# Performance work log

Hardware: AMD Instinct MI355X
Metric: run time of the kernel (lower is better)

Reference implementation:

```python
import jax, jax.numpy as jnp
import numpy as np


def setup_inputs() -> dict:
    key = jax.random.key(0)
    k1, k2, k3, k4 = jax.random.split(key, 4)
    in_features, out_features = 4096, 11008
    n_tokens = 64
    x = jax.random.normal(k1, (n_tokens, in_features), dtype=jnp.float32)
    # int8-valued weights stored as int32 (values in [-128, 127] range subset)
    weight_int = jax.random.randint(k2, (out_features, in_features), 0, 127, dtype=jnp.int32)
    weight_scale = jnp.float32(0.01)
    weight_zero_point = 3  # scalar int zero point
    bias = jax.random.normal(k3, (out_features,), dtype=jnp.float32) * 0.02
    return {
        "x": x,
        "weight_int": weight_int,
        "weight_scale": weight_scale,
        "weight_zero_point": weight_zero_point,
        "bias": bias,
    }


def reference(x, weight_int, weight_scale, weight_zero_point, bias):
    # Dequantize: W = (W_int - zp) * scale, shape [out, in]
    w = (weight_int.astype(jnp.float32) - jnp.float32(weight_zero_point)) * weight_scale
    # F.linear: y = x @ W^T + b
    out = jnp.einsum("ti,oi->to", x, w)
    return out + bias
```

## Files before the change

### kernel.cpp

```cpp
#include <hip/hip_runtime.h>
#include <hip/hip_bf16.h>

typedef __attribute__((ext_vector_type(8))) short short8;
typedef __attribute__((ext_vector_type(4))) float f32x4;
typedef __attribute__((ext_vector_type(4))) int   int4v;

#define IN_F   4096
#define OUT_F  11008
#define KSPLIT 4
#define KPART  (IN_F / KSPLIT)
#define BK     64
#define NIT    (KPART / BK)
#define DEPTH  3

__device__ __forceinline__ short bf16_rne(float f) {
    unsigned u = __builtin_bit_cast(unsigned, f);
    u += 0x7FFFu + ((u >> 16) & 1u);
    return (short)(u >> 16);
}

__device__ __forceinline__ void gld16(const void* g, void* l) {
    __builtin_amdgcn_global_load_lds(
        (const __attribute__((address_space(1))) unsigned int*)g,
        (__attribute__((address_space(3))) unsigned int*)l,
        16, 0, 0);
}

__device__ __forceinline__ short8 deq8(int4v q0, int4v q1, int zp) {
    short8 r;
#pragma unroll
    for (int j = 0; j < 4; ++j) {
        r[j]     = (short)(__builtin_bit_cast(unsigned, (float)(q0[j] - zp)) >> 16);
        r[j + 4] = (short)(__builtin_bit_cast(unsigned, (float)(q1[j] - zp)) >> 16);
    }
    return r;
}

__global__ __launch_bounds__(256)
void xcast(const float* __restrict__ x, unsigned short* __restrict__ xb) {
    const int i = (blockIdx.x * 256 + threadIdx.x) * 8;
    f32x4 a = *(const f32x4*)(x + i);
    f32x4 b = *(const f32x4*)(x + i + 4);
    short8 o;
#pragma unroll
    for (int j = 0; j < 4; ++j) { o[j] = bf16_rne(a[j]); o[j + 4] = bf16_rne(b[j]); }
    *(short8*)(xb + i) = o;
}

__global__ __launch_bounds__(256)
void binit(const float* __restrict__ bias, float* __restrict__ out) {
    const unsigned cid = blockIdx.x * 256 + threadIdx.x;
    const unsigned row = cid / (OUT_F / 8);
    const unsigned o   = (cid - row * (OUT_F / 8)) * 8;
    f32x4 b0 = *(const f32x4*)(bias + o);
    f32x4 b1 = *(const f32x4*)(bias + o + 4);
    float* dst = out + (size_t)row * OUT_F + o;
    *(f32x4*)dst = b0;
    *(f32x4*)(dst + 4) = b1;
}

#define STAGE(IT) do {                                                        \
    const int _s = (IT) % DEPTH;                                              \
    const int* _wsi = wsrc + (size_t)(IT) * BK;                               \
    gld16(_wsi,              (char*)wt[_s] + tid * 16);                       \
    gld16(_wsi + 16 * IN_F,  (char*)wt[_s] + 4096  + tid * 16);               \
    gld16(_wsi + 32 * IN_F,  (char*)wt[_s] + 8192  + tid * 16);               \
    gld16(_wsi + 48 * IN_F,  (char*)wt[_s] + 12288 + tid * 16);               \
    const unsigned short* _xsi = xsrc + (size_t)(IT) * BK;                    \
    gld16(_xsi,            (char*)xt[_s] + tid * 16);                         \
    gld16(_xsi + 32 * IN_F, (char*)xt[_s] + 4096 + tid * 16);                 \
} while (0)

#define COMPUTE(S) do {                                                       \
    const char* _wb = (const char*)wt[S] + wrow_off;                          \
    int4v _q00 = *(const int4v*)(_wb + cw00);                                 \
    int4v _q01 = *(const int4v*)(_wb + cw01);                                 \
    int4v _q10 = *(const int4v*)(_wb + cw10);                                 \
    int4v _q11 = *(const int4v*)(_wb + cw11);                                 \
    short8 _B0 = deq8(_q00, _q01, zp);                                        \
    short8 _B1 = deq8(_q10, _q11, zp);                                        \
    const char* _xb = (const char*)xt[S] + arow;                              \
    short8 _a;                                                                \
    _a = *(const short8*)(_xb +        ca0);                                  \
    acc0 = __builtin_amdgcn_mfma_f32_16x16x32_bf16(_a, _B0, acc0, 0, 0, 0);   \
    _a = *(const short8*)(_xb +        ca1);                                  \
    acc0 = __builtin_amdgcn_mfma_f32_16x16x32_bf16(_a, _B1, acc0, 0, 0, 0);   \
    _a = *(const short8*)(_xb + 2048 + ca0);                                  \
    acc1 = __builtin_amdgcn_mfma_f32_16x16x32_bf16(_a, _B0, acc1, 0, 0, 0);   \
    _a = *(const short8*)(_xb + 2048 + ca1);                                  \
    acc1 = __builtin_amdgcn_mfma_f32_16x16x32_bf16(_a, _B1, acc1, 0, 0, 0);   \
    _a = *(const short8*)(_xb + 4096 + ca0);                                  \
    acc2 = __builtin_amdgcn_mfma_f32_16x16x32_bf16(_a, _B0, acc2, 0, 0, 0);   \
    _a = *(const short8*)(_xb + 4096 + ca1);                                  \
    acc2 = __builtin_amdgcn_mfma_f32_16x16x32_bf16(_a, _B1, acc2, 0, 0, 0);   \
    _a = *(const short8*)(_xb + 6144 + ca0);                                  \
    acc3 = __builtin_amdgcn_mfma_f32_16x16x32_bf16(_a, _B0, acc3, 0, 0, 0);   \
    _a = *(const short8*)(_xb + 6144 + ca1);                                  \
    acc3 = __builtin_amdgcn_mfma_f32_16x16x32_bf16(_a, _B1, acc3, 0, 0, 0);   \
} while (0)

__global__ __launch_bounds__(256, 2)
void qlin6(const unsigned short* __restrict__ xb, const int* __restrict__ w,
           const float* __restrict__ scale_p, const int* __restrict__ zp_p,
           float* __restrict__ out)
{
    __shared__ __align__(16) int            wt[DEPTH][64 * BK];
    __shared__ __align__(16) unsigned short xt[DEPTH][64 * BK];

    const int tid  = threadIdx.x;
    const int lane = tid & 63;
    const int wv   = tid >> 6;
    const int l15  = lane & 15;
    const int lg   = lane >> 4;

    const int ob = blockIdx.x >> 2;
    const int kh = blockIdx.x & 3;
    const int o0 = ob * 64;
    const int kb = kh * KPART;

    const int   zp    = zp_p[0];
    const float scale = scale_p[0];

    const int wr = tid >> 4;
    const int wc = (tid & 15) ^ (wr & 7);
    const int* wsrc = w + (size_t)(o0 + wr) * IN_F + kb + wc * 4;

    const int xr = tid >> 3;
    const int xc = (tid & 7) ^ (xr & 7);
    const unsigned short* xsrc = xb + (size_t)xr * IN_F + kb + xc * 8;

    const int rswz = l15 & 7;
    const int wrow_off = (wv * 16 + l15) * 256;
    const int cw00 = ((lg * 2    ) ^ rswz) * 16;
    const int cw01 = ((lg * 2 + 1) ^ rswz) * 16;
    const int cw10 = ((8 + lg * 2    ) ^ rswz) * 16;
    const int cw11 = ((8 + lg * 2 + 1) ^ rswz) * 16;
    const int arow = l15 * 128;
    const int ca0  = ((lg    ) ^ rswz) * 16;
    const int ca1  = ((4 + lg) ^ rswz) * 16;

    f32x4 acc0 = {0.f, 0.f, 0.f, 0.f};
    f32x4 acc1 = {0.f, 0.f, 0.f, 0.f};
    f32x4 acc2 = {0.f, 0.f, 0.f, 0.f};
    f32x4 acc3 = {0.f, 0.f, 0.f, 0.f};

    STAGE(0);
    STAGE(1);

#pragma unroll 3
    for (int it = 0; it < NIT - 1; ++it) {
        asm volatile("s_waitcnt vmcnt(6)" ::: "memory");
        __builtin_amdgcn_s_barrier();
        if (it + 2 < NIT) STAGE(it + 2);
        COMPUTE(it % DEPTH);
    }
    asm volatile("s_waitcnt vmcnt(0)" ::: "memory");
    __builtin_amdgcn_s_barrier();
    COMPUTE((NIT - 1) % DEPTH);

    {
        const int o = o0 + wv * 16 + l15;
        float* op = out + o;
#pragma unroll
        for (int r = 0; r < 4; ++r) {
            const int tr = lg * 4 + r;
            unsafeAtomicAdd(op + (size_t)(tr     ) * OUT_F, scale * acc0[r]);
            unsafeAtomicAdd(op + (size_t)(tr + 16) * OUT_F, scale * acc1[r]);
            unsafeAtomicAdd(op + (size_t)(tr + 32) * OUT_F, scale * acc2[r]);
            unsafeAtomicAdd(op + (size_t)(tr + 48) * OUT_F, scale * acc3[r]);
        }
    }
}

extern "C" void kernel_launch(void* const* d_in, const int* in_sizes, int n_in,
                              void* d_out, int out_size, void* d_ws, size_t ws_size,
                              hipStream_t stream) {
    const float* x     = (const float*)d_in[0];
    const int*   w     = (const int*)d_in[1];
    const float* scale = (const float*)d_in[2];
    const int*   zp    = (const int*)d_in[3];
    const float* bias  = (const float*)d_in[4];
    float*       out   = (float*)d_out;
    unsigned short* xbf = (unsigned short*)d_ws;

    xcast<<<dim3(128), dim3(256), 0, stream>>>(x, xbf);
    binit<<<dim3(344), dim3(256), 0, stream>>>(bias, out);
    qlin6<<<dim3((OUT_F / 64) * KSPLIT), dim3(256), 0, stream>>>(xbf, w, scale, zp, out);
}
```

Before: 47.97 us.

## Widen output tile to 128 columns, split K eight ways, merge prep kernels

Each block now runs 512 threads over 128 output columns, so one x tile staged in shared memory serves twice as many weight rows. K is split eight ways instead of four, giving more blocks for the weight stream. The shared-memory pipeline drops from triple to double buffering, with an extra barrier before each refill. The x cast and bias init are merged into one prep kernel, saving a launch. In exchange the kernel issues twice as many float atomics to the output, uses more shared memory per block, and has shorter K loops.

```diff
diff --git a/kernel.cpp b/kernel.cpp
--- a/kernel.cpp
+++ b/kernel.cpp
@@ -7,11 +7,12 @@
 
 #define IN_F   4096
 #define OUT_F  11008
-#define KSPLIT 4
+#define COLS   128
+#define KSPLIT 8
 #define KPART  (IN_F / KSPLIT)
 #define BK     64
 #define NIT    (KPART / BK)
-#define DEPTH  3
+#define DEPTH  2
 
 __device__ __forceinline__ short bf16_rne(float f) {
     unsigned u = __builtin_bit_cast(unsigned, f);
@@ -37,19 +38,18 @@
 }
 
 __global__ __launch_bounds__(256)
-void xcast(const float* __restrict__ x, unsigned short* __restrict__ xb) {
-    const int i = (blockIdx.x * 256 + threadIdx.x) * 8;
-    f32x4 a = *(const f32x4*)(x + i);
-    f32x4 b = *(const f32x4*)(x + i + 4);
-    short8 o;
+void prep(const float* __restrict__ x, const float* __restrict__ bias,
+          unsigned short* __restrict__ xb, float* __restrict__ out) {
+    const unsigned cid = blockIdx.x * 256 + threadIdx.x;
+    if (blockIdx.x < 128) {
+        const int i = cid * 8;
+        f32x4 a = *(const f32x4*)(x + i);
+        f32x4 b = *(const f32x4*)(x + i + 4);
+        short8 o;
 #pragma unroll
-    for (int j = 0; j < 4; ++j) { o[j] = bf16_rne(a[j]); o[j + 4] = bf16_rne(b[j]); }
-    *(short8*)(xb + i) = o;
-}
-
-__global__ __launch_bounds__(256)
-void binit(const float* __restrict__ bias, float* __restrict__ out) {
-    const unsigned cid = blockIdx.x * 256 + threadIdx.x;
+        for (int j = 0; j < 4; ++j) { o[j] = bf16_rne(a[j]); o[j + 4] = bf16_rne(b[j]); }
+        *(short8*)(xb + i) = o;
+    }
     const unsigned row = cid / (OUT_F / 8);
     const unsigned o   = (cid - row * (OUT_F / 8)) * 8;
     f32x4 b0 = *(const f32x4*)(bias + o);
@@ -60,15 +60,13 @@
 }
 
 #define STAGE(IT) do {                                                        \
-    const int _s = (IT) % DEPTH;                                              \
+    const int _s = (IT) & (DEPTH - 1);                                        \
     const int* _wsi = wsrc + (size_t)(IT) * BK;                               \
-    gld16(_wsi,              (char*)wt[_s] + tid * 16);                       \
-    gld16(_wsi + 16 * IN_F,  (char*)wt[_s] + 4096  + tid * 16);               \
-    gld16(_wsi + 32 * IN_F,  (char*)wt[_s] + 8192  + tid * 16);               \
-    gld16(_wsi + 48 * IN_F,  (char*)wt[_s] + 12288 + tid * 16);               \
-    const unsigned short* _xsi = xsrc + (size_t)(IT) * BK;                    \
-    gld16(_xsi,            (char*)xt[_s] + tid * 16);                         \
-    gld16(_xsi + 32 * IN_F, (char*)xt[_s] + 4096 + tid * 16);                 \
+    gld16(_wsi,             (char*)wt[_s] + tid * 16);                        \
+    gld16(_wsi + 32 * IN_F, (char*)wt[_s] + 8192  + tid * 16);                \
+    gld16(_wsi + 64 * IN_F, (char*)wt[_s] + 16384 + tid * 16);                \
+    gld16(_wsi + 96 * IN_F, (char*)wt[_s] + 24576 + tid * 16);                \
+    gld16(xsrc + (size_t)(IT) * BK, (char*)xt[_s] + tid * 16);                \
 } while (0)
 
 #define COMPUTE(S) do {                                                       \
@@ -99,12 +97,12 @@
     acc3 = __builtin_amdgcn_mfma_f32_16x16x32_bf16(_a, _B1, acc3, 0, 0, 0);   \
 } while (0)
 
-__global__ __launch_bounds__(256, 2)
-void qlin6(const unsigned short* __restrict__ xb, const int* __restrict__ w,
+__global__ __launch_bounds__(512, 4)
+void qlin8(const unsigned short* __restrict__ xb, const int* __restrict__ w,
            const float* __restrict__ scale_p, const int* __restrict__ zp_p,
            float* __restrict__ out)
 {
-    __shared__ __align__(16) int            wt[DEPTH][64 * BK];
+    __shared__ __align__(16) int            wt[DEPTH][COLS * BK];
     __shared__ __align__(16) unsigned short xt[DEPTH][64 * BK];
 
     const int tid  = threadIdx.x;
@@ -113,9 +111,9 @@
     const int l15  = lane & 15;
     const int lg   = lane >> 4;
 
-    const int ob = blockIdx.x >> 2;
-    const int kh = blockIdx.x & 3;
-    const int o0 = ob * 64;
+    const int ob = blockIdx.x >> 3;
+    const int kh = blockIdx.x & 7;
+    const int o0 = ob * COLS;
     const int kb = kh * KPART;
 
     const int   zp    = zp_p[0];
@@ -147,16 +145,17 @@
     STAGE(0);
     STAGE(1);
 
-#pragma unroll 3
-    for (int it = 0; it < NIT - 1; ++it) {
-        asm volatile("s_waitcnt vmcnt(6)" ::: "memory");
+#pragma unroll
+    for (int it = 0; it < NIT; ++it) {
+        if (it < NIT - 1) asm volatile("s_waitcnt vmcnt(5)" ::: "memory");
+        else              asm volatile("s_waitcnt vmcnt(0)" ::: "memory");
         __builtin_amdgcn_s_barrier();
-        if (it + 2 < NIT) STAGE(it + 2);
-        COMPUTE(it % DEPTH);
+        COMPUTE(it & 1);
+        if (it + 2 < NIT) {
+            __builtin_amdgcn_s_barrier();
+            STAGE(it + 2);
+        }
     }
-    asm volatile("s_waitcnt vmcnt(0)" ::: "memory");
-    __builtin_amdgcn_s_barrier();
-    COMPUTE((NIT - 1) % DEPTH);
 
     {
         const int o = o0 + wv * 16 + l15;
@@ -183,7 +182,6 @@
     float*       out   = (float*)d_out;
     unsigned short* xbf = (unsigned short*)d_ws;
 
-    xcast<<<dim3(128), dim3(256), 0, stream>>>(x, xbf);
-    binit<<<dim3(344), dim3(256), 0, stream>>>(bias, out);
-    qlin6<<<dim3((OUT_F / 64) * KSPLIT), dim3(256), 0, stream>>>(xbf, w, scale, zp, out);
+    prep<<<dim3(344), dim3(256), 0, stream>>>(x, bias, xbf, out);
+    qlin8<<<dim3((OUT_F / COLS) * KSPLIT), dim3(512), 0, stream>>>(xbf, w, scale, zp, out);
 }
```

Result: no change. 48.32 us (median of 2 runs) (+0.7%).
